# Performance work log

Hardware: AMD Instinct MI355X
Metric: run time of the kernel (lower is better)

## Reference

```python
import jax, jax.numpy as jnp
import numpy as np

BITS = 8
KH, KW = 3, 3
STRIDE = (1, 1)
PAD = (1, 1)


def _quantize_signed_symmetric(x, bits=BITS):
    # Per-tensor symmetric quantization: scale = max|x| / qmax, q = clip(round(x/scale)).
    qmax = float(2 ** (bits - 1) - 1)
    scale = jnp.max(jnp.abs(x)) / qmax
    q = jnp.clip(jnp.round(x / scale), -qmax, qmax)
    return q, scale


def _unfold(x, kh, kw, stride, pad):
    # torch.nn.functional.unfold: output [B, C*kh*kw, Hout*Wout], feature order (c, kh, kw).
    B, C, H, W = x.shape
    sh, sw = stride
    ph, pw = pad
    Hout = (H + 2 * ph - kh) // sh + 1
    Wout = (W + 2 * pw - kw) // sw + 1
    xp = jnp.pad(x, ((0, 0), (0, 0), (ph, ph), (pw, pw)))
    patches = []
    for i in range(kh):  # small fixed loop over kernel taps (9 iters)
        for j in range(kw):
            patches.append(
                xp[:, :, i:i + (Hout - 1) * sh + 1:sh, j:j + (Wout - 1) * sw + 1:sw]
            )
    # [B, C, kh*kw, Hout, Wout] -> [B, C*kh*kw, Hout*Wout]
    p = jnp.stack(patches, axis=2)
    return p.reshape(B, C * kh * kw, Hout * Wout), Hout, Wout


def setup_inputs() -> dict:
    key = jax.random.key(0)
    k1, k2, k3 = jax.random.split(key, 3)
    x = jax.random.normal(k1, (8, 32, 224, 224), dtype=jnp.float32)
    weight = jax.random.normal(k2, (32, 32, 3, 3), dtype=jnp.float32)
    bias = jax.random.normal(k3, (32,), dtype=jnp.float32)
    return {"x": x, "weight": weight, "bias": bias}


def reference(x, weight, bias):
    Cout = weight.shape[0]
    B = x.shape[0]
    qw, w_scale = _quantize_signed_symmetric(weight)           # values are exact small ints
    x_unf, Hout, Wout = _unfold(x, KH, KW, STRIDE, PAD)        # [B, K, L], K=Cin*kh*kw
    qx, x_scale = _quantize_signed_symmetric(x_unf)
    qw_flat = qw.reshape(Cout, -1)                             # [Cout, K]
    # Integer GEMM done in fp32: |sum| <= K*127^2 = 288*16129 < 2^24, so exact.
    out = jnp.einsum("ok,bkl->bol", qw_flat, qx)               # [B, Cout, L]
    out = out * (x_scale * w_scale)                            # dequantize
    out = out + bias[None, :, None]
    return out.reshape(B, Cout, Hout, Wout)
```

## Files before the change

kernel.cpp:

```cpp
#include <hip/hip_runtime.h>
#include <hip/hip_bf16.h>
#include <stdint.h>


typedef int i32x4  __attribute__((ext_vector_type(4)));
typedef int i32x16 __attribute__((ext_vector_type(16)));

#define CIN   32
#define COUT  32
#define HH    224
#define WW    224
#define NB    8
#define QMAXF 127.0f
#define PP    226

#define RED_BLOCKS 1024
#define PF_OFF  16
#define QW_OFF  8192
#define QX_OFF  32768


__global__ __launch_bounds__(256) void k_prep(const float* __restrict__ x, int n4,
                                              const float* __restrict__ wgt,
                                              unsigned* __restrict__ ws) {
    const int tid = threadIdx.x;
    __shared__ float red[4];
    if (blockIdx.x < RED_BLOCKS) {
        const float4* x4 = (const float4*)x;
        float m = 0.f;
        for (int i = blockIdx.x * 256 + tid; i < n4; i += RED_BLOCKS * 256) {
            float4 v = x4[i];
            m = fmaxf(m, fmaxf(fmaxf(fabsf(v.x), fabsf(v.y)), fmaxf(fabsf(v.z), fabsf(v.w))));
        }
        #pragma unroll
        for (int off = 32; off >= 1; off >>= 1) m = fmaxf(m, __shfl_xor(m, off));
        if ((tid & 63) == 0) red[tid >> 6] = m;
        __syncthreads();
        if (tid == 0)
            ((float*)ws)[PF_OFF + blockIdx.x] =
                fmaxf(fmaxf(red[0], red[1]), fmaxf(red[2], red[3]));
    } else {
        float m = 0.f;
        for (int i = tid; i < COUT * CIN * 9; i += 256) m = fmaxf(m, fabsf(wgt[i]));
        #pragma unroll
        for (int off = 32; off >= 1; off >>= 1) m = fmaxf(m, __shfl_xor(m, off));
        if ((tid & 63) == 0) red[tid >> 6] = m;
        __syncthreads();
        const float mw = fmaxf(fmaxf(red[0], red[1]), fmaxf(red[2], red[3]));
        const float wscale = mw / QMAXF;
        if (tid == 0) ws[1] = __float_as_uint(wscale);
        signed char* qw = (signed char*)ws + QW_OFF;
        for (int e = tid; e < COUT * 288; e += 256) {
            const int co = e / 288, k = e % 288;
            const int t = k >> 5, ci = k & 31;
            const int kh = t / 3, kw = t % 3;
            const float v = wgt[((co * CIN + ci) * 3 + kh) * 3 + kw];
            float q = rintf(v / wscale);
            q = fminf(fmaxf(q, -QMAXF), QMAXF);
            qw[e] = (signed char)(int)q;
        }
    }
}

__global__ __launch_bounds__(256) void k_quant(const float* __restrict__ x,
                                               unsigned* __restrict__ ws,
                                               signed char* __restrict__ qx) {
    __shared__ float red[4];
    const float* pf = (const float*)ws + PF_OFF;
    float m = 0.f;
    for (int i = threadIdx.x; i < RED_BLOCKS; i += 256) m = fmaxf(m, pf[i]);
    #pragma unroll
    for (int off = 32; off >= 1; off >>= 1) m = fmaxf(m, __shfl_xor(m, off));
    if ((threadIdx.x & 63) == 0) red[threadIdx.x >> 6] = m;
    __syncthreads();
    const float xscale =
        fmaxf(fmaxf(red[0], red[1]), fmaxf(red[2], red[3])) / QMAXF;
    if (blockIdx.x == 0 && threadIdx.x == 0) ws[0] = __float_as_uint(xscale);

    const int total = NB * PP * PP * 2;
    for (int o16 = blockIdx.x * 256 + threadIdx.x; o16 < total; o16 += gridDim.x * 256) {
        const int half = o16 & 1;
        int t = o16 >> 1;
        const int wp = t % PP; t /= PP;
        const int hp = t % PP;
        const int b  = t / PP;
        union { signed char c[16]; int4 v; } u;
        u.v = make_int4(0, 0, 0, 0);
        if (hp != 0 && hp != PP - 1 && wp != 0 && wp != PP - 1) {
            const float* xp =
                x + ((size_t)(b * CIN + half * 16) * HH + (hp - 1)) * WW + (wp - 1);
            #pragma unroll
            for (int c = 0; c < 16; ++c) {
                const float v = xp[c * (HH * WW)];
                float q = rintf(v / xscale);
                q = fminf(fmaxf(q, -QMAXF), QMAXF);
                u.c[c] = (signed char)(int)q;
            }
        }
        ((int4*)qx)[o16] = u.v;
    }
}

__global__ __launch_bounds__(256) void k_conv(const signed char* __restrict__ qx,
                                              const signed char* __restrict__ qw,
                                              const float* __restrict__ bias,
                                              const unsigned* __restrict__ ws,
                                              float* __restrict__ out) {
    const int tid  = threadIdx.x;
    const int lane = tid & 63;
    const int wv   = tid >> 6;
    const int w0   = (blockIdx.x % 7) * 32;
    const int hb   = ((blockIdx.x / 7) % 28) * 8;
    const int b    = blockIdx.x / (7 * 28);
    const int h    = hb + wv * 2;
    const int col  = lane & 31;
    const int hi   = lane >> 5;

    const float s = __uint_as_float(ws[0]) * __uint_as_float(ws[1]);

    i32x4 afr[9];
    #pragma unroll
    for (int t = 0; t < 9; ++t)
        afr[t] = *(const i32x4*)&qw[col * 288 + t * 32 + hi * 16];

    i32x16 acc0 = {0,0,0,0,0,0,0,0,0,0,0,0,0,0,0,0};
    i32x16 acc1 = {0,0,0,0,0,0,0,0,0,0,0,0,0,0,0,0};

    const signed char* base =
        qx + (((size_t)b * PP + h) * PP + (w0 + col)) * CIN + hi * 16;
    #pragma unroll
    for (int pr = 0; pr < 4; ++pr) {
        #pragma unroll
        for (int kw = 0; kw < 3; ++kw) {
            const i32x4 bf = *(const i32x4*)(base + (pr * PP + kw) * CIN);
            if (pr <= 2)
                acc0 = __builtin_amdgcn_mfma_i32_32x32x32_i8(afr[pr * 3 + kw], bf, acc0, 0, 0, 0);
            if (pr >= 1)
                acc1 = __builtin_amdgcn_mfma_i32_32x32x32_i8(afr[(pr - 1) * 3 + kw], bf, acc1, 0, 0, 0);
        }
    }

    const size_t hw0 = (size_t)h * WW + w0 + col;
    #pragma unroll
    for (int r = 0; r < 16; ++r) {
        const int co = (r & 3) + 8 * (r >> 2) + 4 * hi;
        const float bv = bias[co];
        float* op = out + (size_t)(b * COUT + co) * (HH * WW) + hw0;
        op[0]  = (float)acc0[r] * s + bv;
        op[WW] = (float)acc1[r] * s + bv;
    }
}

extern "C" void kernel_launch(void* const* d_in, const int* in_sizes, int n_in,
                              void* d_out, int out_size, void* d_ws, size_t ws_size,
                              hipStream_t stream) {
    const float* x    = (const float*)d_in[0];
    const float* wgt  = (const float*)d_in[1];
    const float* bias = (const float*)d_in[2];
    float* out        = (float*)d_out;
    unsigned* ws      = (unsigned*)d_ws;
    const signed char* qw = (const signed char*)d_ws + QW_OFF;
    signed char* qx       = (signed char*)d_ws + QX_OFF;

    const int n4 = in_sizes[0] / 4;
    k_prep <<<RED_BLOCKS + 1, 256, 0, stream>>>(x, n4, wgt, ws);
    k_quant<<<3200, 256, 0, stream>>>(x, ws, qx);
    k_conv <<<NB * 28 * 7, 256, 0, stream>>>(qx, qw, bias, ws, out);
}
```

Before: 132.2 us.

## Fuse activation quantization into conv kernel via LDS-staged halo tile

Removes the separate quantization kernel and its int8 padded global intermediate. Each conv block now reads fp32 input for its 10x34 halo tile, quantizes it, packs channels into LDS with a padded stride, and feeds the MFMAs from LDS. This drops a kernel launch and the global write and re-read of the quantized activations. In exchange, halo pixels are re-read and re-quantized by neighbouring blocks, and each block re-reduces the 1024 partial maxima.

```diff
diff --git a/kernel.cpp b/kernel.cpp
--- a/kernel.cpp
+++ b/kernel.cpp
@@ -3,6 +3,7 @@
 #include <stdint.h>
 
 
+typedef int i32x2  __attribute__((ext_vector_type(2)));
 typedef int i32x4  __attribute__((ext_vector_type(4)));
 typedef int i32x16 __attribute__((ext_vector_type(16)));
 
@@ -12,12 +13,15 @@
 #define WW    224
 #define NB    8
 #define QMAXF 127.0f
-#define PP    226
 
 #define RED_BLOCKS 1024
 #define PF_OFF  16
 #define QW_OFF  8192
-#define QX_OFF  32768
+
+#define RT   8
+#define SR   10
+#define SW   34
+#define PXS  10
 
 
 __global__ __launch_bounds__(256) void k_prep(const float* __restrict__ x, int n4,
@@ -62,77 +66,78 @@
     }
 }
 
-__global__ __launch_bounds__(256) void k_quant(const float* __restrict__ x,
-                                               unsigned* __restrict__ ws,
-                                               signed char* __restrict__ qx) {
+__global__ __launch_bounds__(256) void k_fused(const float* __restrict__ x,
+                                               const signed char* __restrict__ qw,
+                                               const float* __restrict__ bias,
+                                               const unsigned* __restrict__ ws,
+                                               float* __restrict__ out) {
+    __shared__ int lds[SR * SW * PXS];
     __shared__ float red[4];
-    const float* pf = (const float*)ws + PF_OFF;
-    float m = 0.f;
-    for (int i = threadIdx.x; i < RED_BLOCKS; i += 256) m = fmaxf(m, pf[i]);
-    #pragma unroll
-    for (int off = 32; off >= 1; off >>= 1) m = fmaxf(m, __shfl_xor(m, off));
-    if ((threadIdx.x & 63) == 0) red[threadIdx.x >> 6] = m;
-    __syncthreads();
-    const float xscale =
-        fmaxf(fmaxf(red[0], red[1]), fmaxf(red[2], red[3])) / QMAXF;
-    if (blockIdx.x == 0 && threadIdx.x == 0) ws[0] = __float_as_uint(xscale);
 
-    const int total = NB * PP * PP * 2;
-    for (int o16 = blockIdx.x * 256 + threadIdx.x; o16 < total; o16 += gridDim.x * 256) {
-        const int half = o16 & 1;
-        int t = o16 >> 1;
-        const int wp = t % PP; t /= PP;
-        const int hp = t % PP;
-        const int b  = t / PP;
-        union { signed char c[16]; int4 v; } u;
-        u.v = make_int4(0, 0, 0, 0);
-        if (hp != 0 && hp != PP - 1 && wp != 0 && wp != PP - 1) {
-            const float* xp =
-                x + ((size_t)(b * CIN + half * 16) * HH + (hp - 1)) * WW + (wp - 1);
-            #pragma unroll
-            for (int c = 0; c < 16; ++c) {
-                const float v = xp[c * (HH * WW)];
-                float q = rintf(v / xscale);
-                q = fminf(fmaxf(q, -QMAXF), QMAXF);
-                u.c[c] = (signed char)(int)q;
-            }
-        }
-        ((int4*)qx)[o16] = u.v;
-    }
-}
-
-__global__ __launch_bounds__(256) void k_conv(const signed char* __restrict__ qx,
-                                              const signed char* __restrict__ qw,
-                                              const float* __restrict__ bias,
-                                              const unsigned* __restrict__ ws,
-                                              float* __restrict__ out) {
     const int tid  = threadIdx.x;
     const int lane = tid & 63;
     const int wv   = tid >> 6;
     const int w0   = (blockIdx.x % 7) * 32;
     const int hb   = ((blockIdx.x / 7) % 28) * 8;
     const int b    = blockIdx.x / (7 * 28);
-    const int h    = hb + wv * 2;
     const int col  = lane & 31;
     const int hi   = lane >> 5;
 
-    const float s = __uint_as_float(ws[0]) * __uint_as_float(ws[1]);
+    const float* pf = (const float*)ws + PF_OFF;
+    float m = 0.f;
+    for (int i = tid; i < RED_BLOCKS; i += 256) m = fmaxf(m, pf[i]);
+    #pragma unroll
+    for (int off = 32; off >= 1; off >>= 1) m = fmaxf(m, __shfl_xor(m, off));
+    if ((tid & 63) == 0) red[tid >> 6] = m;
+    __syncthreads();
+    const float xscale =
+        fmaxf(fmaxf(red[0], red[1]), fmaxf(red[2], red[3])) / QMAXF;
+    const float s = xscale * __uint_as_float(ws[1]);
 
     i32x4 afr[9];
     #pragma unroll
     for (int t = 0; t < 9; ++t)
         afr[t] = *(const i32x4*)&qw[col * 288 + t * 32 + hi * 16];
 
+    #pragma unroll
+    for (int it = 0; it < 11; ++it) {
+        const int t = it * 256 + tid;
+        if (t < SR * 8 * SW) {
+            const int px  = t % SW;
+            const int q2  = t / SW;
+            const int ci0 = q2 & 7;
+            const int row = q2 >> 3;
+            const int hg  = hb - 1 + row;
+            const int wg  = w0 - 1 + px;
+            unsigned pack = 0u;
+            if ((unsigned)hg < HH && (unsigned)wg < WW) {
+                const float* xp =
+                    x + ((size_t)(b * CIN + ci0 * 4) * HH + hg) * WW + wg;
+                #pragma unroll
+                for (int j = 0; j < 4; ++j) {
+                    const float v = xp[j * (HH * WW)];
+                    float q = rintf(v / xscale);
+                    q = fminf(fmaxf(q, -QMAXF), QMAXF);
+                    pack |= ((unsigned)((int)q & 0xff)) << (8 * j);
+                }
+            }
+            lds[(row * SW + px) * PXS + ci0] = (int)pack;
+        }
+    }
+    __syncthreads();
+
     i32x16 acc0 = {0,0,0,0,0,0,0,0,0,0,0,0,0,0,0,0};
     i32x16 acc1 = {0,0,0,0,0,0,0,0,0,0,0,0,0,0,0,0};
 
-    const signed char* base =
-        qx + (((size_t)b * PP + h) * PP + (w0 + col)) * CIN + hi * 16;
+    const int r0 = wv * 2;
     #pragma unroll
     for (int pr = 0; pr < 4; ++pr) {
         #pragma unroll
         for (int kw = 0; kw < 3; ++kw) {
-            const i32x4 bf = *(const i32x4*)(base + (pr * PP + kw) * CIN);
+            const int widx = ((r0 + pr) * SW + col + kw) * PXS + hi * 4;
+            const i32x2 lo = *(const i32x2*)&lds[widx];
+            const i32x2 hi2 = *(const i32x2*)&lds[widx + 2];
+            const i32x4 bf = {lo[0], lo[1], hi2[0], hi2[1]};
             if (pr <= 2)
                 acc0 = __builtin_amdgcn_mfma_i32_32x32x32_i8(afr[pr * 3 + kw], bf, acc0, 0, 0, 0);
             if (pr >= 1)
@@ -140,6 +145,7 @@
         }
     }
 
+    const int h = hb + wv * 2;
     const size_t hw0 = (size_t)h * WW + w0 + col;
     #pragma unroll
     for (int r = 0; r < 16; ++r) {
@@ -160,10 +166,8 @@
     float* out        = (float*)d_out;
     unsigned* ws      = (unsigned*)d_ws;
     const signed char* qw = (const signed char*)d_ws + QW_OFF;
-    signed char* qx       = (signed char*)d_ws + QX_OFF;
 
     const int n4 = in_sizes[0] / 4;
     k_prep <<<RED_BLOCKS + 1, 256, 0, stream>>>(x, n4, wgt, ws);
-    k_quant<<<3200, 256, 0, stream>>>(x, ws, qx);
-    k_conv <<<NB * 28 * 7, 256, 0, stream>>>(qx, qw, bias, ws, out);
+    k_fused<<<NB * 28 * 7, 256, 0, stream>>>(x, qw, bias, ws, out);
 }
```

After: 146.6 us. 10.9% more time.
